# Performance work log

Measured on AMD Instinct MI355X. Metric: run time of the kernel, lower is better.

## Reference

```python
import jax, jax.numpy as jnp
import numpy as np

N_NODES = 100000
N_GRAPHS = 64
INPUT_DIM = 512
EMB_DIM = 256


def setup_inputs() -> dict:
    key = jax.random.key(0)
    k_x, k_vw, k_uw, k_ww = jax.random.split(key, 4)
    x = jax.random.normal(k_x, (N_NODES, INPUT_DIM), dtype=jnp.float32)
    # CSR-style segment offsets: B equal-sized graphs covering [0, N)
    ptr = (jnp.arange(N_GRAPHS + 1, dtype=jnp.int64) * (N_NODES // N_GRAPHS)).astype(jnp.int64)
    V_w = jax.random.normal(k_vw, (INPUT_DIM, EMB_DIM), dtype=jnp.float32) * (1.0 / np.sqrt(INPUT_DIM))
    V_b = jnp.zeros((EMB_DIM,), dtype=jnp.float32)
    U_w = jax.random.normal(k_uw, (INPUT_DIM, EMB_DIM), dtype=jnp.float32) * (1.0 / np.sqrt(INPUT_DIM))
    U_b = jnp.zeros((EMB_DIM,), dtype=jnp.float32)
    w_w = jax.random.normal(k_ww, (EMB_DIM, 1), dtype=jnp.float32) * (1.0 / np.sqrt(EMB_DIM))
    w_b = jnp.zeros((1,), dtype=jnp.float32)
    return {"x": x, "ptr": ptr, "V_w": V_w, "V_b": V_b, "U_w": U_w, "U_b": U_b, "w_w": w_w, "w_b": w_b}


def _segment_ids_from_ptr(ptr, n):
    # segment id of node i = index of the segment whose [ptr[j], ptr[j+1]) contains i
    return jnp.searchsorted(ptr, jnp.arange(n, dtype=ptr.dtype), side="right") - 1


def reference(x, ptr, V_w, V_b, U_w, U_b, w_w, w_b):
    num_segments = ptr.shape[0] - 1
    seg = _segment_ids_from_ptr(ptr, x.shape[0])  # [N] int

    A_V = jnp.tanh(x @ V_w + V_b)                  # [N, E]
    A_U = jax.nn.sigmoid(x @ U_w + U_b)            # [N, E]
    att_row = (A_V * A_U) @ w_w + w_b              # [N, 1]

    # per-segment stable softmax over nodes
    s = att_row[:, 0]                              # [N]
    seg_max = jax.ops.segment_max(s, seg, num_segments=num_segments)
    e = jnp.exp(s - seg_max[seg])
    seg_sum = jax.ops.segment_sum(e, seg, num_segments=num_segments)
    att = e / seg_sum[seg]                         # [N]

    # per-segment attention-weighted sum of node features -> [B, D]
    x_graphs = jax.ops.segment_sum(att[:, None] * x, seg, num_segments=num_segments)
    return att[:, None], x_graphs
```

## Files before the change

kernel.cpp:

```cpp
#include <hip/hip_runtime.h>

typedef __attribute__((ext_vector_type(8))) __bf16 bf16x8;
typedef __attribute__((ext_vector_type(4))) float f32x4;

__device__ __forceinline__ void fma4(float4& a, float t, const float4 v) {
    a.x += t * v.x; a.y += t * v.y; a.z += t * v.z; a.w += t * v.w;
}

__global__ __launch_bounds__(256) void prep_weights(
    const float* __restrict__ Vw, const float* __restrict__ Uw,
    __bf16* __restrict__ Wfrag) {
    int id = blockIdx.x * 256 + threadIdx.x;
    int m  = id >> 14;
    int cb = (id >> 10) & 15;
    int kb = (id >> 6) & 15;
    int l  = id & 63;
    int col = cb * 16 + (l & 15);
    int k0  = kb * 32 + (l >> 4) * 8;
    const float* src = (m ? Uw : Vw) + (size_t)k0 * 256 + col;
    bf16x8 p;
#pragma unroll
    for (int j = 0; j < 8; ++j) p[j] = (__bf16)src[j * 256];
    *(bf16x8*)(Wfrag + (size_t)id * 8) = p;
}

__global__ __launch_bounds__(512, 4) void gemm_score(
    const float* __restrict__ x, const __bf16* __restrict__ Wfrag,
    const float* __restrict__ Vb, const float* __restrict__ Ub,
    const float* __restrict__ ww, float* __restrict__ s_out, int M) {
    __shared__ unsigned char lds[2 * 16384];
    const int tid  = threadIdx.x;
    const int row0 = blockIdx.x * 64;
    const int l  = tid & 63;
    const int w  = tid >> 6;
    const int lr = l & 15;
    const int lg = l >> 4;

    const int r0 = tid >> 4;
    const int r1 = r0 + 32;
    const int c16 = tid & 15;
    int g0 = row0 + r0; if (g0 >= M) g0 = M - 1;
    int g1 = row0 + r1; if (g1 >= M) g1 = M - 1;
    const float* src0 = x + (size_t)g0 * 512 + c16 * 8;
    const float* src1 = x + (size_t)g1 * 512 + c16 * 8;
    const unsigned d0 = (unsigned)(r0 * 256 + ((c16 ^ (r0 & 15)) << 4));
    const unsigned d1 = (unsigned)(r1 * 256 + ((c16 ^ (r1 & 15)) << 4));

    float4 f0, f1, f2, f3;
#define LOADC(kc)                                                   \
    {                                                               \
        const float* p0 = src0 + (kc) * 128;                        \
        const float* p1 = src1 + (kc) * 128;                        \
        f0 = *(const float4*)(p0);  f1 = *(const float4*)(p0 + 4);  \
        f2 = *(const float4*)(p1);  f3 = *(const float4*)(p1 + 4);  \
    }
#define STOREC(b)                                                   \
    {                                                               \
        bf16x8 p;                                                   \
        p[0]=(__bf16)f0.x; p[1]=(__bf16)f0.y; p[2]=(__bf16)f0.z;    \
        p[3]=(__bf16)f0.w; p[4]=(__bf16)f1.x; p[5]=(__bf16)f1.y;    \
        p[6]=(__bf16)f1.z; p[7]=(__bf16)f1.w;                       \
        *(bf16x8*)(lds + (b) * 16384 + d0) = p;                     \
        p[0]=(__bf16)f2.x; p[1]=(__bf16)f2.y; p[2]=(__bf16)f2.z;    \
        p[3]=(__bf16)f2.w; p[4]=(__bf16)f3.x; p[5]=(__bf16)f3.y;    \
        p[6]=(__bf16)f3.z; p[7]=(__bf16)f3.w;                       \
        *(bf16x8*)(lds + (b) * 16384 + d1) = p;                     \
    }

    const __bf16* pV0 = Wfrag + (size_t)(2 * w + 0) * 8192 + l * 8;
    const __bf16* pV1 = Wfrag + (size_t)(2 * w + 1) * 8192 + l * 8;
    const __bf16* pU0 = pV0 + 131072;
    const __bf16* pU1 = pV1 + 131072;

    f32x4 aV[4][2], aU[4][2];
#pragma unroll
    for (int mt = 0; mt < 4; ++mt)
#pragma unroll
        for (int nt = 0; nt < 2; ++nt) {
            aV[mt][nt] = (f32x4){0.f, 0.f, 0.f, 0.f};
            aU[mt][nt] = (f32x4){0.f, 0.f, 0.f, 0.f};
        }

    LOADC(0);
    STOREC(0);
    __syncthreads();

#pragma unroll
    for (int kc = 0; kc < 4; ++kc) {
        if (kc < 3) LOADC(kc + 1);
        const unsigned base = (unsigned)((kc & 1) * 16384);
#pragma unroll
        for (int kk = 0; kk < 4; ++kk) {
            bf16x8 a[4];
#pragma unroll
            for (int mt = 0; mt < 4; ++mt) {
                int r = mt * 16 + lr;
                a[mt] = *(const bf16x8*)(lds + base + r * 256 +
                                         ((((kk << 2) + lg) ^ (r & 15)) << 4));
            }
            const int kb = (kc << 2) + kk;
            bf16x8 bv0 = *(const bf16x8*)(pV0 + kb * 512);
            bf16x8 bv1 = *(const bf16x8*)(pV1 + kb * 512);
            bf16x8 bu0 = *(const bf16x8*)(pU0 + kb * 512);
            bf16x8 bu1 = *(const bf16x8*)(pU1 + kb * 512);
#pragma unroll
            for (int mt = 0; mt < 4; ++mt) {
                aV[mt][0] = __builtin_amdgcn_mfma_f32_16x16x32_bf16(a[mt], bv0, aV[mt][0], 0, 0, 0);
                aV[mt][1] = __builtin_amdgcn_mfma_f32_16x16x32_bf16(a[mt], bv1, aV[mt][1], 0, 0, 0);
                aU[mt][0] = __builtin_amdgcn_mfma_f32_16x16x32_bf16(a[mt], bu0, aU[mt][0], 0, 0, 0);
                aU[mt][1] = __builtin_amdgcn_mfma_f32_16x16x32_bf16(a[mt], bu1, aU[mt][1], 0, 0, 0);
            }
        }
        __syncthreads();
        if (kc < 3) { STOREC((kc + 1) & 1); __syncthreads(); }
    }
#undef LOADC
#undef STOREC

    float rowsum[4][4];
#pragma unroll
    for (int mt = 0; mt < 4; ++mt)
#pragma unroll
        for (int r = 0; r < 4; ++r) rowsum[mt][r] = 0.f;

#pragma unroll
    for (int nt = 0; nt < 2; ++nt) {
        int col = w * 32 + nt * 16 + lr;
        float bv = Vb[col];
        float bu = Ub[col];
        float wj = ww[col];
#pragma unroll
        for (int mt = 0; mt < 4; ++mt)
#pragma unroll
            for (int r = 0; r < 4; ++r) {
                float zv = aV[mt][nt][r] + bv;
                float zu = aU[mt][nt][r] + bu;
                float t  = 1.f - 2.f * __builtin_amdgcn_rcpf(__expf(2.f * zv) + 1.f);
                float sg = __builtin_amdgcn_rcpf(1.f + __expf(-zu));
                rowsum[mt][r] += t * sg * wj;
            }
    }

#pragma unroll
    for (int mt = 0; mt < 4; ++mt)
#pragma unroll
        for (int r = 0; r < 4; ++r) {
            float v = rowsum[mt][r];
            v += __shfl_xor(v, 1, 64);
            v += __shfl_xor(v, 2, 64);
            v += __shfl_xor(v, 4, 64);
            v += __shfl_xor(v, 8, 64);
            rowsum[mt][r] = v;
        }

    float* sred = (float*)lds;
    if (lr == 0) {
#pragma unroll
        for (int mt = 0; mt < 4; ++mt)
#pragma unroll
            for (int r = 0; r < 4; ++r)
                sred[w * 64 + mt * 16 + lg * 4 + r] = rowsum[mt][r];
    }
    __syncthreads();
    if (tid < 64) {
        float s = 0.f;
#pragma unroll
        for (int ww_ = 0; ww_ < 8; ++ww_) s += sred[ww_ * 64 + tid];
        int node = row0 + tid;
        if (node < M) s_out[node] = s;
    }
}

__global__ __launch_bounds__(256) void seg_softmax(
    const float* __restrict__ s, const int* __restrict__ ptr,
    float* __restrict__ att, int nseg, int ntot) {
    __shared__ float red[4];
    __shared__ float bmax, bsum;
    int g = blockIdx.x, tid = threadIdx.x;
    int i0 = ptr[g], i1 = ptr[g + 1];
    if (i0 < 0) i0 = 0;  if (i0 > ntot) i0 = ntot;
    if (i1 < i0) i1 = i0; if (i1 > ntot) i1 = ntot;
    int iw1 = (g == nseg - 1) ? ntot : i1;

    float m = -3.4e38f;
    for (int i = i0 + tid; i < i1; i += 256) m = fmaxf(m, s[i]);
    for (int o = 1; o < 64; o <<= 1) m = fmaxf(m, __shfl_xor(m, o, 64));
    if ((tid & 63) == 0) red[tid >> 6] = m;
    __syncthreads();
    if (tid == 0)
        bmax = fmaxf(fmaxf(red[0], red[1]), fmaxf(red[2], red[3]));
    __syncthreads();
    m = bmax;

    float sum = 0.f;
    for (int i = i0 + tid; i < i1; i += 256) sum += __expf(s[i] - m);
    for (int o = 1; o < 64; o <<= 1) sum += __shfl_xor(sum, o, 64);
    if ((tid & 63) == 0) red[tid >> 6] = sum;
    __syncthreads();
    if (tid == 0) bsum = red[0] + red[1] + red[2] + red[3];
    __syncthreads();
    float inv = 1.f / bsum;

    for (int i = i0 + tid; i < iw1; i += 256) att[i] = __expf(s[i] - m) * inv;
}

__global__ __launch_bounds__(512) void seg_weighted_sum(
    const float* __restrict__ x, const float* __restrict__ att,
    const int* __restrict__ ptr, float* __restrict__ xg, int chunks) {
    __shared__ float4 sredv[512];
    const float4* x4 = (const float4*)x;
    int g = blockIdx.x / chunks, c = blockIdx.x % chunks;
    int c4 = threadIdx.x & 127, ro = threadIdx.x >> 7;
    int i0 = ptr[g], i1 = ptr[g + 1];
    int len = i1 - i0;
    int n0 = i0 + (int)(((long long)len * c) / chunks);
    int n1 = i0 + (int)(((long long)len * (c + 1)) / chunks);

    float4 a0 = {0,0,0,0}, a1 = {0,0,0,0}, a2 = {0,0,0,0}, a3 = {0,0,0,0};
    int i = n0 + ro;
    for (; i + 12 < n1; i += 16) {
        float t0 = att[i], t1 = att[i + 4], t2 = att[i + 8], t3 = att[i + 12];
        float4 v0 = x4[(size_t)(i     ) * 128 + c4];
        float4 v1 = x4[(size_t)(i +  4) * 128 + c4];
        float4 v2 = x4[(size_t)(i +  8) * 128 + c4];
        float4 v3 = x4[(size_t)(i + 12) * 128 + c4];
        fma4(a0, t0, v0); fma4(a1, t1, v1); fma4(a2, t2, v2); fma4(a3, t3, v3);
    }
    for (; i < n1; i += 4) fma4(a0, att[i], x4[(size_t)i * 128 + c4]);
    fma4(a0, 1.f, a1); fma4(a2, 1.f, a3); fma4(a0, 1.f, a2);
    sredv[threadIdx.x] = a0;
    __syncthreads();
    if (threadIdx.x < 128) {
        float4 r = sredv[threadIdx.x];
        float4 rb = sredv[threadIdx.x + 128];
        float4 rc = sredv[threadIdx.x + 256];
        float4 rd = sredv[threadIdx.x + 384];
        fma4(r, 1.f, rb); fma4(rc, 1.f, rd); fma4(r, 1.f, rc);
        float* dst = &xg[(size_t)g * 512 + c4 * 4];
        atomicAdd(dst + 0, r.x);
        atomicAdd(dst + 1, r.y);
        atomicAdd(dst + 2, r.z);
        atomicAdd(dst + 3, r.w);
    }
}

extern "C" void kernel_launch(void* const* d_in, const int* in_sizes, int n_in,
                              void* d_out, int out_size, void* d_ws, size_t ws_size,
                              hipStream_t stream) {
    const float* x   = (const float*)d_in[0];
    const int*   ptr = (const int*)d_in[1];
    const float* Vw  = (const float*)d_in[2];
    const float* Vb  = (const float*)d_in[3];
    const float* Uw  = (const float*)d_in[4];
    const float* Ub  = (const float*)d_in[5];
    const float* ww  = (const float*)d_in[6];

    const int M    = in_sizes[0] / 512;
    const int nseg = in_sizes[1] - 1;

    float* att = (float*)d_out;
    float* xg  = (float*)d_out + M;

    __bf16* Wfrag = (__bf16*)d_ws;
    float*  s_all = (float*)(Wfrag + 262144);

    prep_weights<<<128, 256, 0, stream>>>(Vw, Uw, Wfrag);
    gemm_score<<<(M + 63) / 64, 512, 0, stream>>>(x, Wfrag, Vb, Ub, ww, s_all, M);
    seg_softmax<<<nseg, 256, 0, stream>>>(s_all, ptr, att, nseg, M);
    hipMemsetAsync(xg, 0, (size_t)nseg * 512 * sizeof(float), stream);
    const int CH = 16;
    seg_weighted_sum<<<nseg * CH, 512, 0, stream>>>(x, att, ptr, xg, CH);
}
```

Before: 381.4 us.

## Stage full 64x512 x tile in LDS upfront, dropping per-chunk double-buffer syncs

Instead of double-buffering 128-column chunks of x through 32KB of LDS with two barriers per chunk, the kernel loads all four chunks up front (several global loads in flight) into 64KB of LDS, then runs the MFMA loop with no intermediate barriers. This removes six __syncthreads per block and lets more global loads be outstanding at once. The cost is doubled LDS per block, which may reduce occupancy from the 4 blocks/CU hinted by launch bounds, and it loses overlap between loading and MFMA within a block. A barrier is added before reusing LDS for the reduction.

```diff
diff --git a/kernel.cpp b/kernel.cpp
--- a/kernel.cpp
+++ b/kernel.cpp
@@ -28,7 +28,7 @@
     const float* __restrict__ x, const __bf16* __restrict__ Wfrag,
     const float* __restrict__ Vb, const float* __restrict__ Ub,
     const float* __restrict__ ww, float* __restrict__ s_out, int M) {
-    __shared__ unsigned char lds[2 * 16384];
+    __shared__ unsigned char lds[4 * 16384];
     const int tid  = threadIdx.x;
     const int row0 = blockIdx.x * 64;
     const int l  = tid & 63;
@@ -46,26 +46,35 @@
     const unsigned d0 = (unsigned)(r0 * 256 + ((c16 ^ (r0 & 15)) << 4));
     const unsigned d1 = (unsigned)(r1 * 256 + ((c16 ^ (r1 & 15)) << 4));
 
-    float4 f0, f1, f2, f3;
-#define LOADC(kc)                                                   \
-    {                                                               \
-        const float* p0 = src0 + (kc) * 128;                        \
-        const float* p1 = src1 + (kc) * 128;                        \
-        f0 = *(const float4*)(p0);  f1 = *(const float4*)(p0 + 4);  \
-        f2 = *(const float4*)(p1);  f3 = *(const float4*)(p1 + 4);  \
-    }
-#define STOREC(b)                                                   \
+#define LOADC(S, kc)                                                \
+    float4 fa##S = *(const float4*)(src0 + (kc) * 128);             \
+    float4 fb##S = *(const float4*)(src0 + (kc) * 128 + 4);         \
+    float4 fc##S = *(const float4*)(src1 + (kc) * 128);             \
+    float4 fd##S = *(const float4*)(src1 + (kc) * 128 + 4);
+#define STOREC(S, kc)                                               \
     {                                                               \
         bf16x8 p;                                                   \
-        p[0]=(__bf16)f0.x; p[1]=(__bf16)f0.y; p[2]=(__bf16)f0.z;    \
-        p[3]=(__bf16)f0.w; p[4]=(__bf16)f1.x; p[5]=(__bf16)f1.y;    \
-        p[6]=(__bf16)f1.z; p[7]=(__bf16)f1.w;                       \
-        *(bf16x8*)(lds + (b) * 16384 + d0) = p;                     \
-        p[0]=(__bf16)f2.x; p[1]=(__bf16)f2.y; p[2]=(__bf16)f2.z;    \
-        p[3]=(__bf16)f2.w; p[4]=(__bf16)f3.x; p[5]=(__bf16)f3.y;    \
-        p[6]=(__bf16)f3.z; p[7]=(__bf16)f3.w;                       \
-        *(bf16x8*)(lds + (b) * 16384 + d1) = p;                     \
-    }
+        p[0]=(__bf16)fa##S.x; p[1]=(__bf16)fa##S.y;                 \
+        p[2]=(__bf16)fa##S.z; p[3]=(__bf16)fa##S.w;                 \
+        p[4]=(__bf16)fb##S.x; p[5]=(__bf16)fb##S.y;                 \
+        p[6]=(__bf16)fb##S.z; p[7]=(__bf16)fb##S.w;                 \
+        *(bf16x8*)(lds + (kc) * 16384 + d0) = p;                    \
+        p[0]=(__bf16)fc##S.x; p[1]=(__bf16)fc##S.y;                 \
+        p[2]=(__bf16)fc##S.z; p[3]=(__bf16)fc##S.w;                 \
+        p[4]=(__bf16)fd##S.x; p[5]=(__bf16)fd##S.y;                 \
+        p[6]=(__bf16)fd##S.z; p[7]=(__bf16)fd##S.w;                 \
+        *(bf16x8*)(lds + (kc) * 16384 + d1) = p;                    \
+    }
+
+    LOADC(0, 0); LOADC(1, 1);
+    STOREC(0, 0);
+    LOADC(2, 2);
+    STOREC(1, 1);
+    LOADC(3, 3);
+    STOREC(2, 2);
+    STOREC(3, 3);
+#undef LOADC
+#undef STOREC
 
     const __bf16* pV0 = Wfrag + (size_t)(2 * w + 0) * 8192 + l * 8;
     const __bf16* pV1 = Wfrag + (size_t)(2 * w + 1) * 8192 + l * 8;
@@ -81,14 +90,11 @@
             aU[mt][nt] = (f32x4){0.f, 0.f, 0.f, 0.f};
         }
 
-    LOADC(0);
-    STOREC(0);
     __syncthreads();
 
 #pragma unroll
     for (int kc = 0; kc < 4; ++kc) {
-        if (kc < 3) LOADC(kc + 1);
-        const unsigned base = (unsigned)((kc & 1) * 16384);
+        const unsigned base = (unsigned)(kc * 16384);
 #pragma unroll
         for (int kk = 0; kk < 4; ++kk) {
             bf16x8 a[4];
@@ -111,11 +117,7 @@
                 aU[mt][1] = __builtin_amdgcn_mfma_f32_16x16x32_bf16(a[mt], bu1, aU[mt][1], 0, 0, 0);
             }
         }
-        __syncthreads();
-        if (kc < 3) { STOREC((kc + 1) & 1); __syncthreads(); }
-    }
-#undef LOADC
-#undef STOREC
+    }
 
     float rowsum[4][4];
 #pragma unroll
@@ -153,6 +155,7 @@
             rowsum[mt][r] = v;
         }
 
+    __syncthreads();
     float* sred = (float*)lds;
     if (lr == 0) {
 #pragma unroll
```

Result: no change. 375.3 us (-1.6%).
